# Optimization experiments

Hardware: AMD Instinct MI355X
Metric: run time of the kernel (lower is better)

Reference implementation:

```python
import jax, jax.numpy as jnp
import numpy as np

S, U, NMEL, T = 32, 10, 40, 120
H, D = 768, 256


def setup_inputs() -> dict:
    key = jax.random.key(0)
    ks = jax.random.split(key, 16)
    def p(k, shape, scale=0.03):
        return jax.random.normal(k, shape, jnp.float32) * scale
    inp = {"mel": jax.random.normal(ks[0], (S, U, 1, NMEL, T), jnp.float32)}
    in_sizes = [NMEL, H, H]
    for l in range(3):
        inp[f"Wih{l}"] = p(ks[1 + 4 * l], (4 * H, in_sizes[l]))
        inp[f"Whh{l}"] = p(ks[2 + 4 * l], (4 * H, H))
        inp[f"bih{l}"] = p(ks[3 + 4 * l], (4 * H,))
        inp[f"bhh{l}"] = p(ks[4 + 4 * l], (4 * H,))
    inp["Wproj"] = p(ks[13], (D, H))
    inp["bproj"] = p(ks[14], (D,))
    inp["loss_w"] = jnp.array([10.0], jnp.float32)
    inp["loss_b"] = jnp.array([-5.0], jnp.float32)
    return inp


def _lstm_layer(x, Wih, Whh, bih, bhh):
    # x: (B, T, In) -> (B, T, H). PyTorch gate order: i, f, g, o.
    B = x.shape[0]
    Hh = Whh.shape[1]
    h0 = jnp.zeros((B, Hh), x.dtype)
    c0 = jnp.zeros((B, Hh), x.dtype)
    bias = bih + bhh
    def step(carry, xt):
        h, c = carry
        gates = xt @ Wih.T + h @ Whh.T + bias  # (B, 4H)
        i, f, g, o = jnp.split(gates, 4, axis=-1)
        c = jax.nn.sigmoid(f) * c + jax.nn.sigmoid(i) * jnp.tanh(g)
        h = jax.nn.sigmoid(o) * jnp.tanh(c)
        return (h, c), h
    _, hs = jax.lax.scan(step, (h0, c0), jnp.swapaxes(x, 0, 1))  # (T, B, H)
    return jnp.swapaxes(hs, 0, 1)


def _ge2e(d3, w, b):
    # d3: (S, U, D) unit-norm d-vectors; w, b: (1,) scalars.
    s, u, _ = d3.shape
    cent = d3.mean(axis=1)  # (S, D) per-speaker centroids
    # leave-one-out positive centroid: (U*cent - self) / (U-1)
    pos_cent = (cent[:, None, :] * u - d3) / (u - 1)  # (S, U, D)
    # cosine sim with eps=1e-6 (F.cosine_similarity clamps norms)
    na = jnp.maximum(jnp.linalg.norm(d3, axis=-1), 1e-6)
    npc = jnp.maximum(jnp.linalg.norm(pos_cent, axis=-1), 1e-6)
    pos_cos = jnp.sum(d3 * pos_cent, axis=-1) / (na * npc)  # (S, U)
    pos_sim = w[0] * pos_cos + b[0]
    # negative sims vs other speakers' centroids (eps=1e-8 default)
    nd = jnp.maximum(jnp.linalg.norm(d3, axis=-1), 1e-8)  # (S, U)
    nc = jnp.maximum(jnp.linalg.norm(cent, axis=-1), 1e-8)  # (S,)
    all_cos = jnp.einsum('sud,kd->suk', d3, cent) / (nd[..., None] * nc[None, None, :])
    jj = jnp.arange(s - 1)
    idx = jj[None, :] + (jj[None, :] >= jnp.arange(s)[:, None])  # (S, S-1), skips own speaker
    neg_cos = jnp.take_along_axis(all_cos, jnp.broadcast_to(idx[:, None, :], (s, u, s - 1)), axis=2)
    neg_sim = w[0] * neg_cos + b[0]
    # softmax GE2E loss: -pos + log sum exp(neg)
    loss = jnp.mean(-pos_sim + jax.scipy.special.logsumexp(neg_sim, axis=2))
    return loss, pos_sim.mean(), neg_sim.mean()


def reference(mel, Wih0, Whh0, bih0, bhh0, Wih1, Whh1, bih1, bhh1,
              Wih2, Whh2, bih2, bhh2, Wproj, bproj, loss_w, loss_b):
    s, u = mel.shape[0], mel.shape[1]
    x = mel.reshape(s * u, mel.shape[3], mel.shape[4])  # (B, 40, T)
    x = jnp.transpose(x, (0, 2, 1))  # (B, T, 40)
    for (Wih, Whh, bih, bhh) in ((Wih0, Whh0, bih0, bhh0),
                                 (Wih1, Whh1, bih1, bhh1),
                                 (Wih2, Whh2, bih2, bhh2)):
        x = _lstm_layer(x, Wih, Whh, bih, bhh)
    h = x[:, -1, :]  # last time step
    dvec = h @ Wproj.T + bproj
    dvec = dvec / jnp.linalg.norm(dvec, axis=1, keepdims=True)
    d3 = dvec.reshape(s, u, -1)
    return _ge2e(d3, loss_w, loss_b)
```

## Files before the change

kernel.cpp:

```cpp
#include <hip/hip_runtime.h>
#include <math.h>

#define S_    32
#define U_    10
#define B_    320
#define T_    120
#define NMEL_ 40
#define H_    768
#define G4_   3072
#define D_    256
#define XP_   64
#define K0_   (XP_ + H_)
#define K12_  (2 * H_)
#define NP_   4

#define NB0   48
#define NB12  96
#define NBLK  (NB0 + 2 * NB12)

#define SMEM_BYTES 159744

typedef _Float16 half8 __attribute__((ext_vector_type(8)));
typedef float floatx4 __attribute__((ext_vector_type(4)));

__device__ __forceinline__ float sigm(float x) {
  return 1.f / (1.f + __expf(-x));
}
__device__ __forceinline__ float tanh_f(float x) {
  x = fminf(15.f, fmaxf(-15.f, x));
  float e = __expf(2.f * x);
  return (e - 1.f) / (e + 1.f);
}

template <int AUX>
__device__ __forceinline__ void dma16(const void* g, void* l) {
  __builtin_amdgcn_global_load_lds(
      (const __attribute__((address_space(1))) unsigned int*)g,
      (__attribute__((address_space(3))) unsigned int*)l, 16, 0, AUX);
}

template <int N>
__device__ __forceinline__ void waitvm() {
  __builtin_amdgcn_s_waitcnt(0x3FF0 | (N & 0xF) | ((N >> 4) << 14));
}


__global__ void prep_x0(const float* __restrict__ mel, _Float16* __restrict__ x0) {
  int idx = blockIdx.x * 256 + threadIdx.x;
  if (idx >= B_ * T_ * XP_) return;
  int k = idx & (XP_ - 1);
  int t = (idx >> 6) % T_;
  int b = idx / (XP_ * T_);
  float v = (k < NMEL_) ? mel[((size_t)b * NMEL_ + k) * T_ + t] : 0.f;
  x0[idx] = (_Float16)v;
}

__global__ void prep_w0(const float* __restrict__ Wih, const float* __restrict__ Whh,
                        _Float16* __restrict__ Wc) {
  int idx = blockIdx.x * 256 + threadIdx.x;
  if (idx >= G4_ * K0_) return;
  int k = idx % K0_;
  int n = idx / K0_;
  float v = 0.f;
  if (k < NMEL_)      v = Wih[(size_t)n * NMEL_ + k];
  else if (k >= XP_)  v = Whh[(size_t)n * H_ + (k - XP_)];
  Wc[idx] = (_Float16)v;
}

__global__ void prep_w12(const float* __restrict__ Wih, const float* __restrict__ Whh,
                         _Float16* __restrict__ Wc) {
  int idx = blockIdx.x * 256 + threadIdx.x;
  if (idx >= G4_ * K12_) return;
  int k = idx % K12_;
  int n = idx / K12_;
  float v = (k < H_) ? Wih[(size_t)n * H_ + k] : Whh[(size_t)n * H_ + (k - H_)];
  Wc[idx] = (_Float16)v;
}

__global__ void prep_bias(const float* __restrict__ bih, const float* __restrict__ bhh,
                          float* __restrict__ bias) {
  int idx = blockIdx.x * 256 + threadIdx.x;
  if (idx < G4_) bias[idx] = bih[idx] + bhh[idx];
}


__device__ __forceinline__ void wait_group(int* fl, int sp, int lp, int lane) {
  if (lp < 0 || lp > 2) return;
  if (sp < lp || sp > lp + T_ - 1) return;
  const int tgt = (lp == 0) ? NB0 : NB12;
  const int base = (sp * 3 + lp) * 96;
  int spin = 0;
  for (;;) {
    int v0 = (lane < tgt)
                 ? __hip_atomic_load(&fl[base + lane], __ATOMIC_RELAXED,
                                     __HIP_MEMORY_SCOPE_AGENT) : 1;
    int v1 = (lane + 64 < tgt)
                 ? __hip_atomic_load(&fl[base + 64 + lane], __ATOMIC_RELAXED,
                                     __HIP_MEMORY_SCOPE_AGENT) : 1;
    if (__all(v0 != 0 && v1 != 0)) break;
    __builtin_amdgcn_s_sleep(1);
    if (++spin > 2000000) break;
  }
}

template <int NT, int NSTG, int NC, int CSPLIT, int AUXX, int AUXH>
__device__ __forceinline__ void gemm_merged(
    const _Float16* __restrict__ lwW, _Float16* __restrict__ lwA,
    const char* __restrict__ srcX, int strideX,
    const char* __restrict__ srcH, int strideH,
    int m0, int lane, floatx4 (&acc)[2][NT],
    int* __restrict__ flags, int sprev, int layer) {
  const int lr = lane & 15, quad = lane >> 4;
  const int rrow = lane >> 2, rq = lane & 3;
  const int rqs = rq ^ ((rrow >> 1) & 3);
  const size_t ox0 = ((size_t)(m0 + rrow) * strideX + rqs * 8) * 2;
  const size_t ox1 = ((size_t)(m0 + 16 + rrow) * strideX + rqs * 8) * 2;
  const size_t oh0 = ((size_t)(m0 + rrow) * strideH + rqs * 8) * 2;
  const size_t oh1 = ((size_t)(m0 + 16 + rrow) * strideH + rqs * 8) * 2;

  auto issue = [&](int c) {
    const int slot = c % NSTG;
    char* ld = (char*)lwA + ((size_t)slot * 320 + m0) * 64;
    if (c < CSPLIT) {
      const char* g = srcX + (size_t)c * 64;
      dma16<AUXX>(g + ox0, ld);
      dma16<AUXX>(g + ox1, ld + 1024);
    } else {
      const char* g = srcH + (size_t)(c - CSPLIT) * 64;
      dma16<AUXH>(g + oh0, ld);
      dma16<AUXH>(g + oh1, ld + 1024);
    }
  };

#pragma unroll
  for (int p = 0; p < NSTG; ++p) issue(p);

  const int asw = (quad ^ ((lr >> 1) & 3)) * 8;

#pragma unroll
  for (int c = 0; c < NC; ++c) {
    const int rem = NC - 1 - c;
    if (rem >= NSTG - 1)      waitvm<2 * (NSTG - 1)>();
    else if (rem == 1)        waitvm<2>();
    else                      waitvm<0>();
    const int slot = c % NSTG;
    const _Float16* aB = lwA + ((size_t)slot * 320 + m0 + lr) * 32 + asw;
    half8 a0 = *(const half8*)(aB);
    half8 a1 = *(const half8*)(aB + 16 * 32);
    half8 bf[NT];
#pragma unroll
    for (int nt = 0; nt < NT; ++nt)
      bf[nt] = *(const half8*)(lwW +
               ((size_t)(c * NT * 16 + nt * 16 + lr) * 32 + asw));
#pragma unroll
    for (int nt = 0; nt < NT; ++nt) {
      acc[0][nt] = __builtin_amdgcn_mfma_f32_16x16x32_f16(a0, bf[nt], acc[0][nt], 0, 0, 0);
      acc[1][nt] = __builtin_amdgcn_mfma_f32_16x16x32_f16(a1, bf[nt], acc[1][nt], 0, 0, 0);
    }
    if (c + NSTG < NC) {
      if (c + NSTG == CSPLIT)
        wait_group(flags, sprev, layer, lane);
      issue(c + NSTG);
    }
  }
}

__global__ __launch_bounds__(640)
void lstm_persist(const _Float16* __restrict__ x0,
                  const _Float16* __restrict__ Wc0, const _Float16* __restrict__ Wc1,
                  const _Float16* __restrict__ Wc2,
                  const float* __restrict__ bias, _Float16* __restrict__ hbuf,
                  int* __restrict__ flags, int* __restrict__ tick,
                  int* __restrict__ leadDone) {
  extern __shared__ _Float16 lw[];
  const int bid = blockIdx.x;

  int layer, tile, units, K;
  const _Float16* Wsrc;
  if (bid < NB0)            { layer = 0; tile = bid;              units = 16; K = K0_;  Wsrc = Wc0; }
  else if (bid < NB0+NB12)  { layer = 1; tile = bid - NB0;        units = 8;  K = K12_; Wsrc = Wc1; }
  else                      { layer = 2; tile = bid - NB0 - NB12; units = 8;  K = K12_; Wsrc = Wc2; }
  const int nrows = units * 4;
  const int j0 = tile * units;
  _Float16* lwA = lw + (size_t)(K / 32) * nrows * 32;

  unsigned xcc;
  asm volatile("s_getreg_b32 %0, hwreg(HW_REG_XCC_ID)" : "=s"(xcc));
  xcc &= 7;

  {
    const int total = (K / 32) * nrows * 4;
    for (int idx = threadIdx.x; idx < total; idx += 640) {
      int c = idx / (nrows * 4);
      int rem = idx % (nrows * 4);
      int r = rem >> 2;
      int q = rem & 3;
      int grow = (r / units) * H_ + j0 + (r % units);
      half8 v = *(const half8*)(Wsrc + (size_t)grow * K + c * 32 + q * 8);
      int qs = q ^ ((r >> 1) & 3);
      *(half8*)(lw + ((size_t)(c * nrows + r) * 32 + qs * 8)) = v;
    }
  }
  __syncthreads();

  const int lane = threadIdx.x & 63;
  const int wv = threadIdx.x >> 6;
  const int lr = lane & 15;
  const int quad = lane >> 4;
  const int m0 = wv * 32;
  const int m1 = wv * 32 + 16;
  const int j = j0 + ((units == 16) ? lr : (lr & 7));

  const float bI = bias[layer * G4_ + 0 * H_ + j];
  const float bF = bias[layer * G4_ + 1 * H_ + j];
  const float bG = bias[layer * G4_ + 2 * H_ + j];
  const float bO = bias[layer * G4_ + 3 * H_ + j];

  float cst[2][4] = {{0.f, 0.f, 0.f, 0.f}, {0.f, 0.f, 0.f, 0.f}};

  for (int t = 0; t < T_; ++t) {
    const int s = layer + t;
    const int pprev = (s - 1) & (NP_ - 1);
    const int pcur = s & (NP_ - 1);
    const _Float16* hown = hbuf + (size_t)(layer * NP_ + pprev) * B_ * H_;
    _Float16* hout = hbuf + (size_t)(layer * NP_ + pcur) * B_ * H_;

    if (threadIdx.x == 0) {
      if (__hip_atomic_fetch_add(&tick[xcc * 128 + s], 1, __ATOMIC_RELAXED,
                                 __HIP_MEMORY_SCOPE_AGENT) == 0) {
        __builtin_amdgcn_fence(__ATOMIC_ACQUIRE, "agent");
        __hip_atomic_store(&leadDone[xcc * 128 + s], 1, __ATOMIC_RELEASE,
                           __HIP_MEMORY_SCOPE_AGENT);
      }
    }
    if (lane == 0) {
      int spin = 0;
      while (__hip_atomic_load(&leadDone[xcc * 128 + s], __ATOMIC_RELAXED,
                               __HIP_MEMORY_SCOPE_AGENT) == 0) {
        __builtin_amdgcn_s_sleep(1);
        if (++spin > 2000000) break;
      }
    }

    floatx4 acc0[2][4];
    floatx4 acc2[2][2];

    if (layer == 0) {
#pragma unroll
      for (int a = 0; a < 2; ++a)
#pragma unroll
        for (int b = 0; b < 4; ++b) acc0[a][b] = (floatx4){0.f, 0.f, 0.f, 0.f};
      gemm_merged<4, 2, 26, 2, 0, 1>(lw, lwA,
          (const char*)(x0 + (size_t)t * XP_), T_ * XP_,
          (const char*)hown, H_, m0, lane, acc0, flags, s - 1, 0);
    } else {
      wait_group(flags, s - 1, layer - 1, lane);
#pragma unroll
      for (int a = 0; a < 2; ++a)
#pragma unroll
        for (int b = 0; b < 2; ++b) acc2[a][b] = (floatx4){0.f, 0.f, 0.f, 0.f};
      const char* xsrc = (const char*)(hbuf + (size_t)((layer - 1) * NP_ + pprev) * B_ * H_);
      gemm_merged<2, 3, 48, 24, 1, 1>(lw, lwA,
          xsrc, H_, (const char*)hown, H_, m0, lane, acc2, flags, s - 1, layer);
    }

    wait_group(flags, s - 3, layer + 1, lane);

    if (layer == 0) {
#pragma unroll
      for (int mt = 0; mt < 2; ++mt)
#pragma unroll
        for (int r = 0; r < 4; ++r) {
          float iv = acc0[mt][0][r] + bI;
          float fv = acc0[mt][1][r] + bF;
          float gv = acc0[mt][2][r] + bG;
          float ov = acc0[mt][3][r] + bO;
          float cn = sigm(fv) * cst[mt][r] + sigm(iv) * tanh_f(gv);
          cst[mt][r] = cn;
          int m = (mt ? m1 : m0) + quad * 4 + r;
          hout[(size_t)m * H_ + j] = (_Float16)(sigm(ov) * tanh_f(cn));
        }
    } else {
#pragma unroll
      for (int mt = 0; mt < 2; ++mt)
#pragma unroll
        for (int r = 0; r < 4; ++r) {
          float t0 = acc2[mt][0][r], t1 = acc2[mt][1][r];
          float p0 = __shfl_xor(t0, 8, 64);
          float p1 = __shfl_xor(t1, 8, 64);
          bool lo = (lr < 8);
          float iv = (lo ? t0 : p0) + bI;
          float fv = (lo ? p0 : t0) + bF;
          float gv = (lo ? t1 : p1) + bG;
          float ov = (lo ? p1 : t1) + bO;
          float cn = sigm(fv) * cst[mt][r] + sigm(iv) * tanh_f(gv);
          cst[mt][r] = cn;
          if (lo) {
            int m = (mt ? m1 : m0) + quad * 4 + r;
            hout[(size_t)m * H_ + j] = (_Float16)(sigm(ov) * tanh_f(cn));
          }
        }
    }

    __syncthreads();
    if (threadIdx.x == 0)
      __hip_atomic_store(&flags[(s * 3 + layer) * 96 + tile], 1, __ATOMIC_RELEASE,
                         __HIP_MEMORY_SCOPE_AGENT);
  }
}

__global__ void dvec_kernel(const _Float16* __restrict__ hlast, const float* __restrict__ Wproj,
                            const float* __restrict__ bproj, float* __restrict__ d3) {
  const int m = blockIdx.x;
  const int d = threadIdx.x;
  const _Float16* h = hlast + (size_t)m * H_;
  const float* w = Wproj + (size_t)d * H_;
  float acc = bproj[d];
  for (int k = 0; k < H_; k++) acc += (float)h[k] * w[k];
  __shared__ float red[256];
  red[d] = acc * acc;
  __syncthreads();
  for (int off = 128; off > 0; off >>= 1) {
    if (d < off) red[d] += red[d + off];
    __syncthreads();
  }
  float nrm = sqrtf(red[0]);
  d3[(size_t)m * D_ + d] = acc / nrm;
}

__device__ float block_reduce_sum(float x, float* red) {
  const int d = threadIdx.x;
  red[d] = x;
  __syncthreads();
  for (int off = 128; off > 0; off >>= 1) {
    if (d < off) red[d] += red[d + off];
    __syncthreads();
  }
  float r = red[0];
  __syncthreads();
  return r;
}

__global__ void cent_kernel(const float* __restrict__ d3, float* __restrict__ cent,
                            float* __restrict__ ncent) {
  const int sIdx = blockIdx.x;
  const int d = threadIdx.x;
  float acc = 0.f;
  for (int u = 0; u < U_; u++) acc += d3[((size_t)sIdx * U_ + u) * D_ + d];
  acc *= (1.f / U_);
  cent[sIdx * D_ + d] = acc;
  __shared__ float red[256];
  float n2 = block_reduce_sum(acc * acc, red);
  if (d == 0) ncent[sIdx] = fmaxf(sqrtf(n2), 1e-8f);
}

__global__ void ge2e_kernel(const float* __restrict__ d3, const float* __restrict__ cent,
                            const float* __restrict__ ncent, const float* __restrict__ loss_w,
                            const float* __restrict__ loss_b, float* __restrict__ accums) {
  const int p = blockIdx.x;
  const int sIdx = p / U_;
  const int d = threadIdx.x;
  __shared__ float red[256];
  __shared__ float sims[S_];

  const float v = d3[(size_t)p * D_ + d];
  const float cs = cent[sIdx * D_ + d];
  const float pc = (cs * U_ - v) * (1.f / (U_ - 1));

  float nv2 = block_reduce_sum(v * v, red);
  float npc2 = block_reduce_sum(pc * pc, red);
  float dotp = block_reduce_sum(v * pc, red);

  const float w = loss_w[0], b = loss_b[0];
  const float na = fmaxf(sqrtf(nv2), 1e-6f);
  const float npc = fmaxf(sqrtf(npc2), 1e-6f);
  const float pos_sim = w * (dotp / (na * npc)) + b;
  const float nd = fmaxf(sqrtf(nv2), 1e-8f);

  for (int k = 0; k < S_; k++) {
    float dk = block_reduce_sum(v * cent[k * D_ + d], red);
    if (d == 0) sims[k] = w * (dk / (nd * ncent[k])) + b;
  }
  __syncthreads();
  if (d == 0) {
    float mx = -1e30f;
    for (int k = 0; k < S_; k++)
      if (k != sIdx) mx = fmaxf(mx, sims[k]);
    float se = 0.f, sn = 0.f;
    for (int k = 0; k < S_; k++)
      if (k != sIdx) { se += expf(sims[k] - mx); sn += sims[k]; }
    float lse = mx + logf(se);
    atomicAdd(&accums[0], -pos_sim + lse);
    atomicAdd(&accums[1], pos_sim);
    atomicAdd(&accums[2], sn);
  }
}

__global__ void finalize_kernel(const float* __restrict__ accums, float* __restrict__ out) {
  if (threadIdx.x == 0) {
    out[0] = accums[0] / (float)(S_ * U_);
    out[1] = accums[1] / (float)(S_ * U_);
    out[2] = accums[2] / (float)(S_ * U_ * (S_ - 1));
  }
}

extern "C" void kernel_launch(void* const* d_in, const int* in_sizes, int n_in,
                              void* d_out, int out_size, void* d_ws, size_t ws_size,
                              hipStream_t stream) {
  const float* mel = (const float*)d_in[0];
  const float* Wih[3] = {(const float*)d_in[1], (const float*)d_in[5], (const float*)d_in[9]};
  const float* Whh[3] = {(const float*)d_in[2], (const float*)d_in[6], (const float*)d_in[10]};
  const float* bih[3] = {(const float*)d_in[3], (const float*)d_in[7], (const float*)d_in[11]};
  const float* bhh[3] = {(const float*)d_in[4], (const float*)d_in[8], (const float*)d_in[12]};
  const float* Wproj = (const float*)d_in[13];
  const float* bproj = (const float*)d_in[14];
  const float* loss_w = (const float*)d_in[15];
  const float* loss_b = (const float*)d_in[16];
  float* out = (float*)d_out;

  char* ws = (char*)d_ws;
  size_t off = 0;
  auto alloc = [&](size_t bytes) -> void* {
    void* p = ws + off;
    off = (off + bytes + 255) & ~(size_t)255;
    return p;
  };
  _Float16* x0   = (_Float16*)alloc((size_t)B_ * T_ * XP_ * 2);
  _Float16* Wc0  = (_Float16*)alloc((size_t)G4_ * K0_ * 2);
  _Float16* Wc1  = (_Float16*)alloc((size_t)G4_ * K12_ * 2);
  _Float16* Wc2  = (_Float16*)alloc((size_t)G4_ * K12_ * 2);
  float*    bias = (float*)alloc((size_t)3 * G4_ * 4);
  _Float16* hbuf = (_Float16*)alloc((size_t)3 * NP_ * B_ * H_ * 2);
  float*    d3   = (float*)alloc((size_t)B_ * D_ * 4);
  float*    cent = (float*)alloc((size_t)S_ * D_ * 4);
  float*    ncent = (float*)alloc((size_t)S_ * 4);
  float*    accums = (float*)alloc(64);
  int*      flags = (int*)alloc((size_t)(T_ + 3) * 3 * 96 * 4);
  int*      tick  = (int*)alloc((size_t)8 * 128 * 4);
  int*      lead  = (int*)alloc((size_t)8 * 128 * 4);

  hipMemsetAsync(hbuf, 0, (size_t)3 * NP_ * B_ * H_ * 2, stream);
  hipMemsetAsync(accums, 0, 64, stream);
  hipMemsetAsync(flags, 0, (size_t)(T_ + 3) * 3 * 96 * 4, stream);
  hipMemsetAsync(tick, 0, (size_t)8 * 128 * 4, stream);
  hipMemsetAsync(lead, 0, (size_t)8 * 128 * 4, stream);

  prep_x0<<<(B_ * T_ * XP_ + 255) / 256, 256, 0, stream>>>(mel, x0);
  prep_w0<<<(G4_ * K0_ + 255) / 256, 256, 0, stream>>>(Wih[0], Whh[0], Wc0);
  prep_w12<<<(G4_ * K12_ + 255) / 256, 256, 0, stream>>>(Wih[1], Whh[1], Wc1);
  prep_w12<<<(G4_ * K12_ + 255) / 256, 256, 0, stream>>>(Wih[2], Whh[2], Wc2);
  for (int l = 0; l < 3; l++)
    prep_bias<<<(G4_ + 255) / 256, 256, 0, stream>>>(bih[l], bhh[l], bias + l * G4_);

  hipFuncSetAttribute((const void*)lstm_persist,
                      hipFuncAttributeMaxDynamicSharedMemorySize, SMEM_BYTES);
  void* kargs[] = {(void*)&x0, (void*)&Wc0, (void*)&Wc1, (void*)&Wc2,
                   (void*)&bias, (void*)&hbuf, (void*)&flags, (void*)&tick,
                   (void*)&lead};
  hipLaunchCooperativeKernel((const void*)lstm_persist, dim3(NBLK), dim3(640),
                             kargs, SMEM_BYTES, stream);

  const _Float16* hlast = hbuf + (size_t)(2 * NP_ + 1) * B_ * H_;
  dvec_kernel<<<B_, 256, 0, stream>>>(hlast, Wproj, bproj, d3);
  cent_kernel<<<S_, 256, 0, stream>>>(d3, cent, ncent);
  ge2e_kernel<<<B_, 256, 0, stream>>>(d3, cent, ncent, loss_w, loss_b, accums);
  finalize_kernel<<<1, 64, 0, stream>>>(accums, out);
}
```

Measured before the change: 3.331 ms.

## Keep tail weight chunks in registers to free LDS for deeper A-pipeline

For layers 1 and 2, the last 9 K-chunks of the per-block weight slice move from LDS into per-lane registers loaded once at kernel start. Only 39 chunks stay in LDS. The freed LDS lets the activation staging pipeline go from 3 to 4 stages, and the wait-count logic gains a case for it. Launch bounds now request 3 waves per SIMD, which caps register usage while the 18 half8 register tiles add register pressure. That combination risks spills.

```diff
diff --git a/kernel.cpp b/kernel.cpp
--- a/kernel.cpp
+++ b/kernel.cpp
@@ -18,7 +18,10 @@
 #define NB12  96
 #define NBLK  (NB0 + 2 * NB12)
 
-#define SMEM_BYTES 159744
+#define WLDS12 39
+#define NWR12  9
+
+#define SMEM_BYTES 161792
 
 typedef _Float16 half8 __attribute__((ext_vector_type(8)));
 typedef float floatx4 __attribute__((ext_vector_type(4)));
@@ -103,13 +106,14 @@
   }
 }
 
-template <int NT, int NSTG, int NC, int CSPLIT, int AUXX, int AUXH>
+template <int NT, int NSTG, int NC, int CSPLIT, int AUXX, int AUXH, int NWR>
 __device__ __forceinline__ void gemm_merged(
     const _Float16* __restrict__ lwW, _Float16* __restrict__ lwA,
     const char* __restrict__ srcX, int strideX,
     const char* __restrict__ srcH, int strideH,
     int m0, int lane, floatx4 (&acc)[2][NT],
-    int* __restrict__ flags, int sprev, int layer) {
+    int* __restrict__ flags, int sprev, int layer,
+    const half8 (&wreg)[18]) {
   const int lr = lane & 15, quad = lane >> 4;
   const int rrow = lane >> 2, rq = lane & 3;
   const int rqs = rq ^ ((rrow >> 1) & 3);
@@ -141,6 +145,7 @@
   for (int c = 0; c < NC; ++c) {
     const int rem = NC - 1 - c;
     if (rem >= NSTG - 1)      waitvm<2 * (NSTG - 1)>();
+    else if (rem == 2)        waitvm<4>();
     else if (rem == 1)        waitvm<2>();
     else                      waitvm<0>();
     const int slot = c % NSTG;
@@ -148,10 +153,16 @@
     half8 a0 = *(const half8*)(aB);
     half8 a1 = *(const half8*)(aB + 16 * 32);
     half8 bf[NT];
-#pragma unroll
-    for (int nt = 0; nt < NT; ++nt)
-      bf[nt] = *(const half8*)(lwW +
-               ((size_t)(c * NT * 16 + nt * 16 + lr) * 32 + asw));
+    if (NWR > 0 && c >= NC - NWR) {
+#pragma unroll
+      for (int nt = 0; nt < NT; ++nt)
+        bf[nt] = wreg[(c - (NC - NWR)) * NT + nt];
+    } else {
+#pragma unroll
+      for (int nt = 0; nt < NT; ++nt)
+        bf[nt] = *(const half8*)(lwW +
+                 ((size_t)(c * NT * 16 + nt * 16 + lr) * 32 + asw));
+    }
 #pragma unroll
     for (int nt = 0; nt < NT; ++nt) {
       acc[0][nt] = __builtin_amdgcn_mfma_f32_16x16x32_f16(a0, bf[nt], acc[0][nt], 0, 0, 0);
@@ -165,7 +176,7 @@
   }
 }
 
-__global__ __launch_bounds__(640)
+__global__ __launch_bounds__(640, 3)
 void lstm_persist(const _Float16* __restrict__ x0,
                   const _Float16* __restrict__ Wc0, const _Float16* __restrict__ Wc1,
                   const _Float16* __restrict__ Wc2,
@@ -175,21 +186,21 @@
   extern __shared__ _Float16 lw[];
   const int bid = blockIdx.x;
 
-  int layer, tile, units, K;
+  int layer, tile, units, K, wlds;
   const _Float16* Wsrc;
-  if (bid < NB0)            { layer = 0; tile = bid;              units = 16; K = K0_;  Wsrc = Wc0; }
-  else if (bid < NB0+NB12)  { layer = 1; tile = bid - NB0;        units = 8;  K = K12_; Wsrc = Wc1; }
-  else                      { layer = 2; tile = bid - NB0 - NB12; units = 8;  K = K12_; Wsrc = Wc2; }
+  if (bid < NB0)            { layer = 0; tile = bid;              units = 16; K = K0_;  wlds = 26;     Wsrc = Wc0; }
+  else if (bid < NB0+NB12)  { layer = 1; tile = bid - NB0;        units = 8;  K = K12_; wlds = WLDS12; Wsrc = Wc1; }
+  else                      { layer = 2; tile = bid - NB0 - NB12; units = 8;  K = K12_; wlds = WLDS12; Wsrc = Wc2; }
   const int nrows = units * 4;
   const int j0 = tile * units;
-  _Float16* lwA = lw + (size_t)(K / 32) * nrows * 32;
+  _Float16* lwA = lw + (size_t)wlds * nrows * 32;
 
   unsigned xcc;
   asm volatile("s_getreg_b32 %0, hwreg(HW_REG_XCC_ID)" : "=s"(xcc));
   xcc &= 7;
 
   {
-    const int total = (K / 32) * nrows * 4;
+    const int total = wlds * nrows * 4;
     for (int idx = threadIdx.x; idx < total; idx += 640) {
       int c = idx / (nrows * 4);
       int rem = idx % (nrows * 4);
@@ -211,6 +222,19 @@
   const int m1 = wv * 32 + 16;
   const int j = j0 + ((units == 16) ? lr : (lr & 7));
 
+  half8 wreg[18];
+  if (layer != 0) {
+#pragma unroll
+    for (int cc = 0; cc < NWR12; ++cc)
+#pragma unroll
+      for (int nt = 0; nt < 2; ++nt) {
+        int r = nt * 16 + lr;
+        int grow = (r >> 3) * H_ + j0 + (r & 7);
+        wreg[cc * 2 + nt] =
+            *(const half8*)(Wsrc + (size_t)grow * K + (WLDS12 + cc) * 32 + quad * 8);
+      }
+  }
+
   const float bI = bias[layer * G4_ + 0 * H_ + j];
   const float bF = bias[layer * G4_ + 1 * H_ + j];
   const float bG = bias[layer * G4_ + 2 * H_ + j];
@@ -250,9 +274,9 @@
       for (int a = 0; a < 2; ++a)
 #pragma unroll
         for (int b = 0; b < 4; ++b) acc0[a][b] = (floatx4){0.f, 0.f, 0.f, 0.f};
-      gemm_merged<4, 2, 26, 2, 0, 1>(lw, lwA,
+      gemm_merged<4, 2, 26, 2, 0, 1, 0>(lw, lwA,
           (const char*)(x0 + (size_t)t * XP_), T_ * XP_,
-          (const char*)hown, H_, m0, lane, acc0, flags, s - 1, 0);
+          (const char*)hown, H_, m0, lane, acc0, flags, s - 1, 0, wreg);
     } else {
       wait_group(flags, s - 1, layer - 1, lane);
 #pragma unroll
@@ -260,8 +284,8 @@
 #pragma unroll
         for (int b = 0; b < 2; ++b) acc2[a][b] = (floatx4){0.f, 0.f, 0.f, 0.f};
       const char* xsrc = (const char*)(hbuf + (size_t)((layer - 1) * NP_ + pprev) * B_ * H_);
-      gemm_merged<2, 3, 48, 24, 1, 1>(lw, lwA,
-          xsrc, H_, (const char*)hown, H_, m0, lane, acc2, flags, s - 1, layer);
+      gemm_merged<2, 4, 48, 24, 1, 1, NWR12>(lw, lwA,
+          xsrc, H_, (const char*)hown, H_, m0, lane, acc2, flags, s - 1, layer, wreg);
     }
 
     wait_group(flags, s - 3, layer + 1, lane);
```

Result: no change. 3.319 ms (-0.4%).
